# Optimization experiments

Measured on AMD Instinct MI355X. Metric: run time of the kernel, lower is better.

## Reference

```python
import jax, jax.numpy as jnp
import numpy as np

N_USERS = 100000
N_ITEMS = 50000
N = N_USERS + N_ITEMS
EMB = 64
NNZ = 8000000
N_LAYERS = 3


def setup_inputs() -> dict:
    key = jax.random.key(0)
    k1, k2, k3, k4, k5 = jax.random.split(key, 5)
    user_emb = jax.random.normal(k1, (N_USERS, EMB), dtype=jnp.float32) * 0.1
    item_emb = jax.random.normal(k2, (N_ITEMS, EMB), dtype=jnp.float32) * 0.1
    adj_rows = jax.random.randint(k3, (NNZ,), 0, N, dtype=jnp.int32)
    adj_cols = jax.random.randint(k4, (NNZ,), 0, N, dtype=jnp.int32)
    # normalized-adjacency-like small positive values
    adj_vals = jax.random.uniform(k5, (NNZ,), dtype=jnp.float32) * 0.01
    return {
        "user_emb": user_emb,
        "item_emb": item_emb,
        "adj_rows": adj_rows,
        "adj_cols": adj_cols,
        "adj_vals": adj_vals,
    }


def spmm(rows, cols, vals, x):
    # sparse [N,N] @ dense [N,d]: gather source rows, scale, scatter-add to dest
    msgs = vals[:, None] * x[cols]          # [nnz, d]
    return jax.ops.segment_sum(msgs, rows, num_segments=N)  # [N, d]


def reference(user_emb, item_emb, adj_rows, adj_cols, adj_vals):
    ego = jnp.concatenate([user_emb, item_emb], axis=0)  # [N, d]
    acc = ego  # running sum of layer outputs (fused stack+mean)
    for _ in range(N_LAYERS):
        ego = spmm(adj_rows, adj_cols, adj_vals, ego)
        acc = acc + ego
    all_embeddings = acc / jnp.float32(N_LAYERS + 1)
    return all_embeddings[:N_USERS], all_embeddings[N_USERS:]
```

## Files before the change

### kernel.cpp

```cpp
#include <hip/hip_runtime.h>

#define N_USERS 100000
#define N_ITEMS 50000
#define N_TOTAL 150000
#define EMB 64
#define NNZ_CONST 8000000

#define CB_SHIFT 8
#define ROWS_PER_CB 256
#define NCB 586
#define CAP_R 14592
#define EPB 8192

#define VAL_ENC 1638400.0f
#define VAL_DEC 2.3841858e-9f
#define FP8_SCALE 256.0f

typedef unsigned char u8;
typedef unsigned short u16;
typedef unsigned int u32;
typedef unsigned long long u64;
typedef float v2f __attribute__((ext_vector_type(2)));

__device__ __forceinline__ u16 f32_to_bf16(float f) {
    u32 b = __float_as_uint(f);
    b += 0x7FFFu + ((b >> 16) & 1u);
    return (u16)(b >> 16);
}
__device__ __forceinline__ float bf16lo_to_f32(u32 w) {
    return __uint_as_float(w << 16);
}
__device__ __forceinline__ float bf16hi_to_f32(u32 w) {
    return __uint_as_float(w & 0xFFFF0000u);
}
__device__ __forceinline__ u32 pack_bf16x2(float lo, float hi) {
    return ((u32)f32_to_bf16(hi) << 16) | f32_to_bf16(lo);
}
__device__ __forceinline__ u32 pack_fp8x4(float a, float b, float c, float d) {
    u32 r = (u32)__builtin_amdgcn_cvt_pk_fp8_f32(a, b, 0, false);
    r = (u32)__builtin_amdgcn_cvt_pk_fp8_f32(c, d, (int)r, true);
    return r;
}

__global__ void lgcn_init_kernel(const float* __restrict__ user_emb,
                                 const float* __restrict__ item_emb,
                                 float* __restrict__ acc,
                                 u8* __restrict__ ego8) {
    const long total4 = (long)N_TOTAL * EMB / 4;
    long idx = (long)blockIdx.x * blockDim.x + threadIdx.x;
    if (idx >= total4) return;
    long e = idx * 4;
    const long user_elems = (long)N_USERS * EMB;
    float4 v;
    if (e < user_elems) {
        v = *(const float4*)(user_emb + e);
    } else {
        v = *(const float4*)(item_emb + (e - user_elems));
    }
    *(float4*)(acc + e) = v;
    *(u32*)(ego8 + e) = pack_fp8x4(v.x * FP8_SCALE, v.y * FP8_SCALE,
                                   v.z * FP8_SCALE, v.w * FP8_SCALE);
}

__global__ void lgcn_gcinit_kernel(int* __restrict__ gcursor) {
    int t = blockIdx.x * blockDim.x + threadIdx.x;
    if (t < NCB) gcursor[t] = t * CAP_R;
}

__global__ void __launch_bounds__(512) lgcn_part_kernel(
        const int* __restrict__ rows,
        const int* __restrict__ cols,
        const float* __restrict__ vals,
        int* __restrict__ gcursor,
        u32* __restrict__ pairs,
        u8* __restrict__ rl8) {
    __shared__ u32 stage32[EPB];
    __shared__ u8  stage8[EPB];
    __shared__ int lhist[NCB];
    __shared__ int loffs[NCB + 1];
    __shared__ int lcur[NCB];
    __shared__ int gres[NCB];
    const int t = threadIdx.x;
    const long base = (long)blockIdx.x * EPB;
    long rem = (long)NNZ_CONST - base;
    const int n = (rem < EPB) ? (int)rem : EPB;
    const int n4 = n >> 2;

    for (int i = t; i < NCB; i += 512) lhist[i] = 0;
    __syncthreads();

    for (int i4 = t; i4 < n4; i4 += 512) {
        int4 r = *(const int4*)(rows + base + (long)i4 * 4);
        atomicAdd(&lhist[r.x >> CB_SHIFT], 1);
        atomicAdd(&lhist[r.y >> CB_SHIFT], 1);
        atomicAdd(&lhist[r.z >> CB_SHIFT], 1);
        atomicAdd(&lhist[r.w >> CB_SHIFT], 1);
    }
    __syncthreads();

    if (t < 64) {
        int loc[10];
        int s = 0;
        #pragma unroll
        for (int k = 0; k < 10; ++k) {
            int i = t * 10 + k;
            loc[k] = (i < NCB) ? lhist[i] : 0;
            s += loc[k];
        }
        int inc = s;
        #pragma unroll
        for (int d = 1; d < 64; d <<= 1) {
            int u = __shfl_up(inc, d, 64);
            if (t >= d) inc += u;
        }
        int ex = inc - s;
        #pragma unroll
        for (int k = 0; k < 10; ++k) {
            int i = t * 10 + k;
            if (i < NCB) { loffs[i] = ex; lcur[i] = ex; ex += loc[k]; }
        }
        if (t == 63) loffs[NCB] = ex;
    }
    __syncthreads();

    for (int i = t; i < NCB; i += 512) {
        int c = lhist[i];
        gres[i] = c ? atomicAdd(&gcursor[i], c) : 0;
    }
    __syncthreads();

    for (int i4 = t; i4 < n4; i4 += 512) {
        int4 r = *(const int4*)(rows + base + (long)i4 * 4);
        int4 c = *(const int4*)(cols + base + (long)i4 * 4);
        float4 v = *(const float4*)(vals + base + (long)i4 * 4);
#define PUTL(RR, CC, VV)                                                \
        {                                                               \
            const int cb = (RR) >> CB_SHIFT;                            \
            int pos = atomicAdd(&lcur[cb], 1);                          \
            int k14 = (int)((VV) * VAL_ENC + 0.5f);                     \
            if (k14 > 16383) k14 = 16383;                               \
            stage32[pos] = ((u32)k14 << 18) | (u32)(CC);                \
            stage8[pos] = (u8)((RR) & (ROWS_PER_CB - 1));               \
        }
        PUTL(r.x, c.x, v.x)
        PUTL(r.y, c.y, v.y)
        PUTL(r.z, c.z, v.z)
        PUTL(r.w, c.w, v.w)
#undef PUTL
    }
    __syncthreads();

    for (int i = t; i < n; i += 512) {
        int lo = 0, hi = NCB;
        while (hi - lo > 1) {
            int mid = (lo + hi) >> 1;
            if (loffs[mid] <= i) lo = mid; else hi = mid;
        }
        long d = (long)gres[lo] + (i - loffs[lo]);
        pairs[d] = stage32[i];
        rl8[d] = stage8[i];
    }
}

__global__ void __launch_bounds__(512) lgcn_csort_kernel(
        const int* __restrict__ gcursor,
        const u8* __restrict__ rl8,
        u32* __restrict__ pairs,
        int2* __restrict__ row_rng) {
    __shared__ u32 stage[CAP_R];
    __shared__ int rhist[ROWS_PER_CB];
    __shared__ int roffs[ROWS_PER_CB + 1];
    __shared__ int rcur[ROWS_PER_CB];
    const int b = blockIdx.x;
    const int t = threadIdx.x;
    const long gbase = (long)b * CAP_R;
    int n = gcursor[b] - (int)gbase;
    if (n < 0) n = 0;
    if (n > CAP_R) n = CAP_R;

    if (t < ROWS_PER_CB) rhist[t] = 0;
    __syncthreads();

    for (int i = t; i < n; i += 512)
        atomicAdd(&rhist[rl8[gbase + i]], 1);
    __syncthreads();

    if (t < 64) {
        int l0 = rhist[t * 4 + 0], l1 = rhist[t * 4 + 1];
        int l2 = rhist[t * 4 + 2], l3 = rhist[t * 4 + 3];
        int s = l0 + l1 + l2 + l3;
        int inc = s;
        #pragma unroll
        for (int d = 1; d < 64; d <<= 1) {
            int u = __shfl_up(inc, d, 64);
            if (t >= d) inc += u;
        }
        int ex = inc - s;
        roffs[t * 4 + 0] = ex;
        roffs[t * 4 + 1] = ex + l0;
        roffs[t * 4 + 2] = ex + l0 + l1;
        roffs[t * 4 + 3] = ex + l0 + l1 + l2;
        rcur[t * 4 + 0] = ex;
        rcur[t * 4 + 1] = ex + l0;
        rcur[t * 4 + 2] = ex + l0 + l1;
        rcur[t * 4 + 3] = ex + l0 + l1 + l2;
        if (t == 63) roffs[ROWS_PER_CB] = ex + s;
    }
    __syncthreads();

    if (t < ROWS_PER_CB) {
        int grow = b * ROWS_PER_CB + t;
        if (grow < N_TOTAL)
            row_rng[grow] = make_int2((int)gbase + roffs[t],
                                      (int)gbase + roffs[t + 1]);
    }

    for (int i = t; i < n; i += 512) {
        int rl = rl8[gbase + i];
        int pos = atomicAdd(&rcur[rl], 1);
        stage[pos] = pairs[gbase + i];
    }
    __syncthreads();

    for (int i = t; i < n; i += 512)
        pairs[gbase + i] = stage[i];
}

template <bool WFP8>
__global__ void lgcn_spmm_kernel(const int2* __restrict__ row_rng,
                                 const u32* __restrict__ pairs,
                                 const u8* __restrict__ src8,
                                 u8* __restrict__ dst8,
                                 u16* __restrict__ dst_bf16) {
    const int wave = threadIdx.x >> 6;
    const int lane = threadIdx.x & 63;
    const int grp  = lane >> 3;
    const int l8   = lane & 7;
    const int row = blockIdx.x * 4 + wave;
    if (row >= N_TOTAL) return;
    const int2 rng = row_rng[row];
    const int start = rng.x;
    const int end   = rng.y;

    float4 a0 = make_float4(0.f, 0.f, 0.f, 0.f);
    float4 a1 = make_float4(0.f, 0.f, 0.f, 0.f);
    float4 b0 = make_float4(0.f, 0.f, 0.f, 0.f);
    float4 b1 = make_float4(0.f, 0.f, 0.f, 0.f);

#define PROC(E, Q0, Q1)                                                     \
    {                                                                       \
        const u32 p = __builtin_nontemporal_load(&pairs[E]);                \
        const int   c = (int)(p & 0x3FFFFu);                                \
        const float v = (float)(p >> 18) * VAL_DEC;                         \
        const uint2 x = *(const uint2*)(src8 + (size_t)c * EMB + l8 * 8);   \
        v2f f0 = __builtin_amdgcn_cvt_pk_f32_fp8(x.x, false);               \
        v2f f1 = __builtin_amdgcn_cvt_pk_f32_fp8(x.x, true);                \
        v2f f2 = __builtin_amdgcn_cvt_pk_f32_fp8(x.y, false);               \
        v2f f3 = __builtin_amdgcn_cvt_pk_f32_fp8(x.y, true);                \
        Q0.x += v * f0.x;  Q0.y += v * f0.y;                                \
        Q0.z += v * f1.x;  Q0.w += v * f1.y;                                \
        Q1.x += v * f2.x;  Q1.y += v * f2.y;                                \
        Q1.z += v * f3.x;  Q1.w += v * f3.y;                                \
    }

    int e = start + grp;
    for (; e + 24 < end; e += 32) {
        PROC(e,      a0, a1)
        PROC(e + 8,  b0, b1)
        PROC(e + 16, a0, a1)
        PROC(e + 24, b0, b1)
    }
    for (; e < end; e += 8) {
        PROC(e, a0, a1)
    }
#undef PROC
    a0.x += b0.x; a0.y += b0.y; a0.z += b0.z; a0.w += b0.w;
    a1.x += b1.x; a1.y += b1.y; a1.z += b1.z; a1.w += b1.w;

    #pragma unroll
    for (int m = 8; m <= 32; m <<= 1) {
        a0.x += __shfl_xor(a0.x, m); a0.y += __shfl_xor(a0.y, m);
        a0.z += __shfl_xor(a0.z, m); a0.w += __shfl_xor(a0.w, m);
        a1.x += __shfl_xor(a1.x, m); a1.y += __shfl_xor(a1.y, m);
        a1.z += __shfl_xor(a1.z, m); a1.w += __shfl_xor(a1.w, m);
    }

    if (grp == 0) {
        const size_t o = (size_t)row * EMB + l8 * 8;
        uint4 h;
        h.x = pack_bf16x2(a0.x, a0.y);
        h.y = pack_bf16x2(a0.z, a0.w);
        h.z = pack_bf16x2(a1.x, a1.y);
        h.w = pack_bf16x2(a1.z, a1.w);
        *(uint4*)(dst_bf16 + o) = h;
        if (WFP8) {
            uint2 q;
            q.x = pack_fp8x4(a0.x * FP8_SCALE, a0.y * FP8_SCALE,
                             a0.z * FP8_SCALE, a0.w * FP8_SCALE);
            q.y = pack_fp8x4(a1.x * FP8_SCALE, a1.y * FP8_SCALE,
                             a1.z * FP8_SCALE, a1.w * FP8_SCALE);
            *(uint2*)(dst8 + o) = q;
        }
    }
}

__global__ void lgcn_merge_kernel(float* __restrict__ acc,
                                  const u16* __restrict__ e1,
                                  const u16* __restrict__ e2,
                                  const u16* __restrict__ e3) {
    const long total8 = (long)N_TOTAL * EMB / 8;
    long idx = (long)blockIdx.x * blockDim.x + threadIdx.x;
    if (idx >= total8) return;
    long o = idx * 8;
    float4 x0 = *(const float4*)(acc + o);
    float4 x1 = *(const float4*)(acc + o + 4);
    const uint4 h1 = *(const uint4*)(e1 + o);
    const uint4 h2 = *(const uint4*)(e2 + o);
    const uint4 h3 = *(const uint4*)(e3 + o);
    x0.x = (x0.x + bf16lo_to_f32(h1.x) + bf16lo_to_f32(h2.x) + bf16lo_to_f32(h3.x)) * 0.25f;
    x0.y = (x0.y + bf16hi_to_f32(h1.x) + bf16hi_to_f32(h2.x) + bf16hi_to_f32(h3.x)) * 0.25f;
    x0.z = (x0.z + bf16lo_to_f32(h1.y) + bf16lo_to_f32(h2.y) + bf16lo_to_f32(h3.y)) * 0.25f;
    x0.w = (x0.w + bf16hi_to_f32(h1.y) + bf16hi_to_f32(h2.y) + bf16hi_to_f32(h3.y)) * 0.25f;
    x1.x = (x1.x + bf16lo_to_f32(h1.z) + bf16lo_to_f32(h2.z) + bf16lo_to_f32(h3.z)) * 0.25f;
    x1.y = (x1.y + bf16hi_to_f32(h1.z) + bf16hi_to_f32(h2.z) + bf16hi_to_f32(h3.z)) * 0.25f;
    x1.z = (x1.z + bf16lo_to_f32(h1.w) + bf16lo_to_f32(h2.w) + bf16lo_to_f32(h3.w)) * 0.25f;
    x1.w = (x1.w + bf16hi_to_f32(h1.w) + bf16hi_to_f32(h2.w) + bf16hi_to_f32(h3.w)) * 0.25f;
    *(float4*)(acc + o) = x0;
    *(float4*)(acc + o + 4) = x1;
}

extern "C" void kernel_launch(void* const* d_in, const int* in_sizes, int n_in,
                              void* d_out, int out_size, void* d_ws, size_t ws_size,
                              hipStream_t stream) {
    const float* user_emb = (const float*)d_in[0];
    const float* item_emb = (const float*)d_in[1];
    const int*   adj_rows = (const int*)d_in[2];
    const int*   adj_cols = (const int*)d_in[3];
    const float* adj_vals = (const float*)d_in[4];

    float* acc = (float*)d_out;

    char* ws = (char*)d_ws;
    u8* fp8A = (u8*)ws;             ws += (size_t)N_TOTAL * EMB;
    u8* fp8B = (u8*)ws;             ws += (size_t)N_TOTAL * EMB;
    u16* e1 = (u16*)ws;             ws += (size_t)N_TOTAL * EMB * 2;
    u16* e2 = (u16*)ws;             ws += (size_t)N_TOTAL * EMB * 2;
    u16* e3 = (u16*)ws;             ws += (size_t)N_TOTAL * EMB * 2;
    u32* pairs = (u32*)ws;          ws += (size_t)NCB * CAP_R * 4;
    u8* rl8 = (u8*)ws;              ws += (size_t)NCB * CAP_R;
    int2* row_rng = (int2*)ws;      ws += (size_t)(N_TOTAL + 16) * 8;
    int* gcursor = (int*)ws;        ws += (size_t)(NCB + 8) * 4;

    const int block = 256;
    const long total4 = (long)N_TOTAL * EMB / 4;
    const int grid_elem = (int)((total4 + block - 1) / block);

    lgcn_init_kernel<<<grid_elem, block, 0, stream>>>(user_emb, item_emb, acc, fp8A);

    lgcn_gcinit_kernel<<<(NCB + 255) / 256, 256, 0, stream>>>(gcursor);
    const int grid_part = (NNZ_CONST + EPB - 1) / EPB;
    lgcn_part_kernel<<<grid_part, 512, 0, stream>>>(adj_rows, adj_cols, adj_vals,
                                                    gcursor, pairs, rl8);
    lgcn_csort_kernel<<<NCB, 512, 0, stream>>>(gcursor, rl8, pairs, row_rng);

    const int grid_spmm = (N_TOTAL + 3) / 4;
    lgcn_spmm_kernel<true><<<grid_spmm, block, 0, stream>>>(row_rng, pairs, fp8A, fp8B, e1);
    lgcn_spmm_kernel<true><<<grid_spmm, block, 0, stream>>>(row_rng, pairs, fp8B, fp8A, e2);
    lgcn_spmm_kernel<false><<<grid_spmm, block, 0, stream>>>(row_rng, pairs, fp8A, fp8B, e3);

    const long total8 = (long)N_TOTAL * EMB / 8;
    const int grid_merge = (int)((total8 + block - 1) / block);
    lgcn_merge_kernel<<<grid_merge, block, 0, stream>>>(acc, e1, e2, e3);
}
```

Measured before the change: 504.7 us.

## Pre-sort each row block's edges by column bin before row bucketing

The per-block counting sort first buckets edges by a coarse column bin (low 18 bits of the pair shifted by 10) in shared memory, then does the row scatter from that ordering. Because the atomic slot claims roughly preserve input order, edges within each row should come out grouped by column, which would improve gather locality of source embeddings in the later SpMM passes. The cost is an extra histogram, scan and scatter pass plus about twice the shared memory, which lowers occupancy of the sort kernel.

```diff
diff --git a/kernel.cpp b/kernel.cpp
--- a/kernel.cpp
+++ b/kernel.cpp
@@ -11,6 +11,7 @@
 #define NCB 586
 #define CAP_R 14592
 #define EPB 8192
+#define CBIN 147
 
 #define VAL_ENC 1638400.0f
 #define VAL_DEC 2.3841858e-9f
@@ -167,7 +168,11 @@
         const u8* __restrict__ rl8,
         u32* __restrict__ pairs,
         int2* __restrict__ row_rng) {
-    __shared__ u32 stage[CAP_R];
+    __shared__ u32 stageA[CAP_R];
+    __shared__ u8  rlA[CAP_R];
+    __shared__ u32 stageB[CAP_R];
+    __shared__ int chist[CBIN];
+    __shared__ int ccur[CBIN];
     __shared__ int rhist[ROWS_PER_CB];
     __shared__ int roffs[ROWS_PER_CB + 1];
     __shared__ int rcur[ROWS_PER_CB];
@@ -178,11 +183,44 @@
     if (n < 0) n = 0;
     if (n > CAP_R) n = CAP_R;
 
+    for (int i = t; i < CBIN; i += 512) chist[i] = 0;
     if (t < ROWS_PER_CB) rhist[t] = 0;
     __syncthreads();
 
     for (int i = t; i < n; i += 512)
-        atomicAdd(&rhist[rl8[gbase + i]], 1);
+        atomicAdd(&chist[(pairs[gbase + i] & 0x3FFFFu) >> 10], 1);
+    __syncthreads();
+
+    if (t < 64) {
+        int l0 = 0, l1 = 0, l2 = 0;
+        int i0 = t * 3;
+        if (i0 + 0 < CBIN) l0 = chist[i0 + 0];
+        if (i0 + 1 < CBIN) l1 = chist[i0 + 1];
+        if (i0 + 2 < CBIN) l2 = chist[i0 + 2];
+        int s = l0 + l1 + l2;
+        int inc = s;
+        #pragma unroll
+        for (int d = 1; d < 64; d <<= 1) {
+            int u = __shfl_up(inc, d, 64);
+            if (t >= d) inc += u;
+        }
+        int ex = inc - s;
+        if (i0 + 0 < CBIN) ccur[i0 + 0] = ex;
+        if (i0 + 1 < CBIN) ccur[i0 + 1] = ex + l0;
+        if (i0 + 2 < CBIN) ccur[i0 + 2] = ex + l0 + l1;
+    }
+    __syncthreads();
+
+    for (int i = t; i < n; i += 512) {
+        u32 p = pairs[gbase + i];
+        int pos = atomicAdd(&ccur[(p & 0x3FFFFu) >> 10], 1);
+        stageA[pos] = p;
+        rlA[pos] = rl8[gbase + i];
+    }
+    __syncthreads();
+
+    for (int i = t; i < n; i += 512)
+        atomicAdd(&rhist[rlA[i]], 1);
     __syncthreads();
 
     if (t < 64) {
@@ -216,14 +254,14 @@
     }
 
     for (int i = t; i < n; i += 512) {
-        int rl = rl8[gbase + i];
+        int rl = rlA[i];
         int pos = atomicAdd(&rcur[rl], 1);
-        stage[pos] = pairs[gbase + i];
+        stageB[pos] = stageA[i];
     }
     __syncthreads();
 
     for (int i = t; i < n; i += 512)
-        pairs[gbase + i] = stage[i];
+        pairs[gbase + i] = stageB[i];
 }
 
 template <bool WFP8>
```

New measurement: 527.1 us. 1.04x slower.

## Assign 16 lanes per output row in SpMM and use packed FMA

Applied to the files above, without the earlier changes.

The SpMM kernel now maps each row to 16 lanes (two groups of 8) instead of a full 64-lane wave, so one wave handles four rows. With about 53 nonzeros per row, this should cut idle lanes and reduce the cross-lane shuffle reduction from three rounds to one. Accumulation switches to packed v2f multiply-adds on the fp8-converted pairs. Each row now has less memory-level parallelism, and the tail iterations diverge more when rows inside a wave differ in length.

```diff
diff --git a/kernel.cpp b/kernel.cpp
--- a/kernel.cpp
+++ b/kernel.cpp
@@ -232,73 +232,68 @@
                                  const u8* __restrict__ src8,
                                  u8* __restrict__ dst8,
                                  u16* __restrict__ dst_bf16) {
-    const int wave = threadIdx.x >> 6;
     const int lane = threadIdx.x & 63;
-    const int grp  = lane >> 3;
-    const int l8   = lane & 7;
-    const int row = blockIdx.x * 4 + wave;
+    const int g   = (lane >> 3) & 1;
+    const int l8  = lane & 7;
+    const int row = blockIdx.x * 16 + (threadIdx.x >> 4);
     if (row >= N_TOTAL) return;
     const int2 rng = row_rng[row];
     const int start = rng.x;
     const int end   = rng.y;
 
-    float4 a0 = make_float4(0.f, 0.f, 0.f, 0.f);
-    float4 a1 = make_float4(0.f, 0.f, 0.f, 0.f);
-    float4 b0 = make_float4(0.f, 0.f, 0.f, 0.f);
-    float4 b1 = make_float4(0.f, 0.f, 0.f, 0.f);
-
-#define PROC(E, Q0, Q1)                                                     \
+    const u8* srcl = src8 + l8 * 8;
+
+    v2f qa0 = {0.f, 0.f}, qa1 = {0.f, 0.f}, qa2 = {0.f, 0.f}, qa3 = {0.f, 0.f};
+    v2f qb0 = {0.f, 0.f}, qb1 = {0.f, 0.f}, qb2 = {0.f, 0.f}, qb3 = {0.f, 0.f};
+
+#define PROC(E, Q0, Q1, Q2, Q3)                                             \
     {                                                                       \
         const u32 p = __builtin_nontemporal_load(&pairs[E]);                \
         const int   c = (int)(p & 0x3FFFFu);                                \
         const float v = (float)(p >> 18) * VAL_DEC;                         \
-        const uint2 x = *(const uint2*)(src8 + (size_t)c * EMB + l8 * 8);   \
-        v2f f0 = __builtin_amdgcn_cvt_pk_f32_fp8(x.x, false);               \
-        v2f f1 = __builtin_amdgcn_cvt_pk_f32_fp8(x.x, true);                \
-        v2f f2 = __builtin_amdgcn_cvt_pk_f32_fp8(x.y, false);               \
-        v2f f3 = __builtin_amdgcn_cvt_pk_f32_fp8(x.y, true);                \
-        Q0.x += v * f0.x;  Q0.y += v * f0.y;                                \
-        Q0.z += v * f1.x;  Q0.w += v * f1.y;                                \
-        Q1.x += v * f2.x;  Q1.y += v * f2.y;                                \
-        Q1.z += v * f3.x;  Q1.w += v * f3.y;                                \
-    }
-
-    int e = start + grp;
-    for (; e + 24 < end; e += 32) {
-        PROC(e,      a0, a1)
-        PROC(e + 8,  b0, b1)
-        PROC(e + 16, a0, a1)
-        PROC(e + 24, b0, b1)
-    }
-    for (; e < end; e += 8) {
-        PROC(e, a0, a1)
+        const uint2 x = *(const uint2*)(srcl + ((size_t)c << 6));           \
+        const v2f vv = {v, v};                                              \
+        Q0 += vv * __builtin_amdgcn_cvt_pk_f32_fp8(x.x, false);             \
+        Q1 += vv * __builtin_amdgcn_cvt_pk_f32_fp8(x.x, true);              \
+        Q2 += vv * __builtin_amdgcn_cvt_pk_f32_fp8(x.y, false);             \
+        Q3 += vv * __builtin_amdgcn_cvt_pk_f32_fp8(x.y, true);              \
+    }
+
+    int e = start + g;
+    for (; e + 6 < end; e += 8) {
+        PROC(e,     qa0, qa1, qa2, qa3)
+        PROC(e + 2, qb0, qb1, qb2, qb3)
+        PROC(e + 4, qa0, qa1, qa2, qa3)
+        PROC(e + 6, qb0, qb1, qb2, qb3)
+    }
+    for (; e < end; e += 2) {
+        PROC(e, qa0, qa1, qa2, qa3)
     }
 #undef PROC
-    a0.x += b0.x; a0.y += b0.y; a0.z += b0.z; a0.w += b0.w;
-    a1.x += b1.x; a1.y += b1.y; a1.z += b1.z; a1.w += b1.w;
-
-    #pragma unroll
-    for (int m = 8; m <= 32; m <<= 1) {
-        a0.x += __shfl_xor(a0.x, m); a0.y += __shfl_xor(a0.y, m);
-        a0.z += __shfl_xor(a0.z, m); a0.w += __shfl_xor(a0.w, m);
-        a1.x += __shfl_xor(a1.x, m); a1.y += __shfl_xor(a1.y, m);
-        a1.z += __shfl_xor(a1.z, m); a1.w += __shfl_xor(a1.w, m);
-    }
-
-    if (grp == 0) {
+    qa0 += qb0; qa1 += qb1; qa2 += qb2; qa3 += qb3;
+
+    float s0 = qa0.x, s1 = qa0.y, s2 = qa1.x, s3 = qa1.y;
+    float s4 = qa2.x, s5 = qa2.y, s6 = qa3.x, s7 = qa3.y;
+    s0 += __shfl_xor(s0, 8); s1 += __shfl_xor(s1, 8);
+    s2 += __shfl_xor(s2, 8); s3 += __shfl_xor(s3, 8);
+    s4 += __shfl_xor(s4, 8); s5 += __shfl_xor(s5, 8);
+    s6 += __shfl_xor(s6, 8); s7 += __shfl_xor(s7, 8);
+
+    if (g == 0) {
         const size_t o = (size_t)row * EMB + l8 * 8;
-        uint4 h;
-        h.x = pack_bf16x2(a0.x, a0.y);
-        h.y = pack_bf16x2(a0.z, a0.w);
-        h.z = pack_bf16x2(a1.x, a1.y);
-        h.w = pack_bf16x2(a1.z, a1.w);
-        *(uint4*)(dst_bf16 + o) = h;
+        uint2 h0, h1;
+        h0.x = pack_bf16x2(s0, s1);
+        h0.y = pack_bf16x2(s2, s3);
+        h1.x = pack_bf16x2(s4, s5);
+        h1.y = pack_bf16x2(s6, s7);
+        *(uint2*)(dst_bf16 + o) = h0;
+        *(uint2*)(dst_bf16 + o + 4) = h1;
         if (WFP8) {
             uint2 q;
-            q.x = pack_fp8x4(a0.x * FP8_SCALE, a0.y * FP8_SCALE,
-                             a0.z * FP8_SCALE, a0.w * FP8_SCALE);
-            q.y = pack_fp8x4(a1.x * FP8_SCALE, a1.y * FP8_SCALE,
-                             a1.z * FP8_SCALE, a1.w * FP8_SCALE);
+            q.x = pack_fp8x4(s0 * FP8_SCALE, s1 * FP8_SCALE,
+                             s2 * FP8_SCALE, s3 * FP8_SCALE);
+            q.y = pack_fp8x4(s4 * FP8_SCALE, s5 * FP8_SCALE,
+                             s6 * FP8_SCALE, s7 * FP8_SCALE);
             *(uint2*)(dst8 + o) = q;
         }
     }
@@ -363,7 +358,7 @@
                                                     gcursor, pairs, rl8);
     lgcn_csort_kernel<<<NCB, 512, 0, stream>>>(gcursor, rl8, pairs, row_rng);
 
-    const int grid_spmm = (N_TOTAL + 3) / 4;
+    const int grid_spmm = (N_TOTAL + 15) / 16;
     lgcn_spmm_kernel<true><<<grid_spmm, block, 0, stream>>>(row_rng, pairs, fp8A, fp8B, e1);
     lgcn_spmm_kernel<true><<<grid_spmm, block, 0, stream>>>(row_rng, pairs, fp8B, fp8A, e2);
     lgcn_spmm_kernel<false><<<grid_spmm, block, 0, stream>>>(row_rng, pairs, fp8A, fp8B, e3);
```

New measurement: 508.3 us. Within noise of the previous version (+0.7%).
